# Kernel tuning notes

Measured on AMD Instinct MI355X. Metric: run time of the kernel, lower is better.

The kernel has to match this reference:

```python
import jax, jax.numpy as jnp
import numpy as np
from jax import lax

EPS = 1e-5

def setup_inputs() -> dict:
    key = jax.random.key(0)
    k1, k2 = jax.random.split(key)
    x = jax.random.normal(k1, (8, 256, 64, 64), dtype=jnp.float32)
    W = jax.random.normal(k2, (128, 256, 5, 5), dtype=jnp.float32) * 0.02
    gamma = jnp.ones((128,), dtype=jnp.float32)
    beta = jnp.zeros((128,), dtype=jnp.float32)
    return {"x": x, "W": W, "gamma": gamma, "beta": beta}

def reference(x, W, gamma, beta):
    B, C, H, Wd = x.shape
    # bilinear x2 upsample, half-pixel centers (== torch align_corners=False)
    up = jax.image.resize(x, (B, C, 2 * H, 2 * Wd), method="bilinear")
    # conv2d, stride 1, padding 2, no bias (norm == 'BN')
    out = lax.conv_general_dilated(
        up, W, window_strides=(1, 1), padding=[(2, 2), (2, 2)],
        dimension_numbers=("NCHW", "OIHW", "NCHW"))
    # BatchNorm2d (batch statistics, training-style refresh)
    mean = jnp.mean(out, axis=(0, 2, 3))
    var = jnp.var(out, axis=(0, 2, 3))
    inv = gamma / jnp.sqrt(var + EPS)
    out = (out - mean[None, :, None, None]) * inv[None, :, None, None] + beta[None, :, None, None]
    # activation: torch.relu
    return jax.nn.relu(out)
```

## Files before the change

### kernel.cpp

```cpp
#include <hip/hip_runtime.h>
#include <hip/hip_bf16.h>
#include <stdint.h>

typedef short s8v __attribute__((ext_vector_type(8)));
typedef float f4v __attribute__((ext_vector_type(4)));

__device__ __forceinline__ void async_copy16(const void* gsrc, void* lds_dst) {
  __builtin_amdgcn_global_load_lds(
      (const __attribute__((address_space(1))) uint32_t*)(uintptr_t)gsrc,
      (__attribute__((address_space(3))) uint32_t*)(uint32_t)(uintptr_t)lds_dst,
      16, 0, 0);
}

__global__ void wpack_kernel(const float* __restrict__ W, __hip_bfloat16* __restrict__ Wr) {
  int i = blockIdx.x * 256 + threadIdx.x;
  int ci = i & 255;
  int rest = i >> 8;
  int co = rest & 127;
  int pos = rest >> 7;
  Wr[i] = __float2bfloat16(W[(co * 256 + ci) * 25 + pos]);
}

__global__ __launch_bounds__(256, 2) void upsample_kernel(const float* __restrict__ x,
                                                          __hip_bfloat16* __restrict__ up) {
  __shared__ __hip_bfloat16 lx[10 * 48 * 66];
  const int tid = threadIdx.x;
  const int bx = blockIdx.x;
  const int owb = bx & 1;
  const int ohb = (bx >> 1) & 7;
  const int cb = (bx >> 4) & 3;
  const int b = bx >> 6;
  const int oh0 = ohb * 16, ow0 = owb * 64, c0 = cb * 64;
  const int ih0 = (oh0 >> 1) - 1;
  const int iw_lo = (ow0 >> 1) - 1;
  const int aligned = (iw_lo < 0 ? 0 : iw_lo) & ~15;

  for (int i = tid; i < 64 * 10 * 12; i += 256) {
    int c = i / 120;
    int rem = i - c * 120;
    int r = rem / 12;
    int w4 = (rem - r * 12) * 4;
    int gr = ih0 + r;
    gr = gr < 0 ? 0 : (gr > 63 ? 63 : gr);
    const float4 v = *(const float4*)&x[(((b * 256 + c0 + c) * 64) + gr) * 64 + aligned + w4];
    int base = (r * 48 + w4) * 66 + c;
    lx[base]       = __float2bfloat16(v.x);
    lx[base + 66]  = __float2bfloat16(v.y);
    lx[base + 132] = __float2bfloat16(v.z);
    lx[base + 198] = __float2bfloat16(v.w);
  }
  __syncthreads();

  const int c_l = tid & 63;
  const int owq = tid >> 6;
  for (int it = 0; it < 256; ++it) {
    int oh_l = it >> 4;
    int ow_l = (it & 15) * 4 + owq;
    int oh = oh0 + oh_l, ow = ow0 + ow_l;
    int ihA = (oh >> 1) - ((oh & 1) ^ 1);
    float wh = (oh & 1) ? 0.75f : 0.25f;
    int iwA = (ow >> 1) - ((ow & 1) ^ 1);
    float wwt = (ow & 1) ? 0.75f : 0.25f;
    int r0 = ihA - ih0;
    int w0 = (iwA < 0 ? 0 : iwA) - aligned;
    int w1t = iwA + 1; w1t = w1t > 63 ? 63 : w1t;
    int w1 = w1t - aligned;
    float t00 = __bfloat162float(lx[(r0 * 48 + w0) * 66 + c_l]);
    float t01 = __bfloat162float(lx[(r0 * 48 + w1) * 66 + c_l]);
    float t10 = __bfloat162float(lx[((r0 + 1) * 48 + w0) * 66 + c_l]);
    float t11 = __bfloat162float(lx[((r0 + 1) * 48 + w1) * 66 + c_l]);
    float v = wh * (wwt * t00 + (1.f - wwt) * t01) + (1.f - wh) * (wwt * t10 + (1.f - wwt) * t11);
    up[(((size_t)(b * 128 + oh) * 128) + ow) * 256 + c0 + c_l] = __float2bfloat16(v);
  }
}

#define SLOTC 1056
__global__ __launch_bounds__(512, 2) void conv_kernel(const __hip_bfloat16* __restrict__ up,
                                                      const __hip_bfloat16* __restrict__ Wr,
                                                      float* __restrict__ out,
                                                      float* __restrict__ gstats) {
  __shared__ __align__(16) unsigned short lA[6 * 132 * 64];
  __shared__ __align__(16) unsigned short lB[2][128 * 64];

  const int tid = threadIdx.x;
  const int lane = tid & 63;
  const int wave = tid >> 6;
  const int wm = wave >> 1;
  const int wn = wave & 1;
  const int lane15 = lane & 15;
  const int quad = lane >> 4;
  const int wb = wave << 6;

  const int bid = blockIdx.x;
  const int orig = ((bid & 7) << 5) | (bid >> 3);
  const int b = orig >> 5;
  const int oh0 = (orig & 31) << 2;

  const f4v zero4 = {0.f, 0.f, 0.f, 0.f};

  if (tid < 192) {
    int s = tid >> 5, j = tid & 31;
    int rsel = j >> 3;
    int r = (rsel < 2) ? rsel : (128 + rsel);
    *(f4v*)&lA[(s * SLOTC + r * 8 + (j & 7)) * 8] = zero4;
  }

  f4v acc[8][4];
#pragma unroll
  for (int i = 0; i < 8; ++i)
#pragma unroll
    for (int j = 0; j < 4; ++j) acc[i][j] = zero4;

  for (int rr = 0; rr < 4; ++rr) {
    int ih = oh0 + rr - 2;
    if ((unsigned)ih < 128u) {
      int sp = ih % 6;
      const __hip_bfloat16* uprow = up + (size_t)(b * 128 + ih) * 128 * 256;
#pragma unroll
      for (int t = 0; t < 2; ++t) {
        int pl = t * 512 + wb + lane;
        int riw = pl >> 3, pc = pl & 7;
        int cq = pc ^ ((riw + 2) & 7);
        async_copy16(uprow + riw * 256 + cq * 8,
                     (void*)&lA[(sp * SLOTC + 16 + t * 512 + wb) * 8]);
      }
    }
  }
#pragma unroll
  for (int t = 0; t < 2; ++t) {
    int pl = t * 512 + wb + lane;
    int n = pl >> 3, pc = pl & 7;
    int cq = pc ^ (n & 7);
    async_copy16(Wr + n * 256 + cq * 8, (void*)&lB[0][(t * 512 + wb) * 8]);
  }
  __syncthreads();

  int buf = 0;
  for (int cb = 0; cb < 4; ++cb) {
    const int c0 = cb << 6;
    for (int kh = 0; kh < 5; ++kh) {
      const int ih = oh0 + wm + kh - 2;
      const bool rowok = (unsigned)ih < 128u;
      const int abase = rowok ? (ih % 6) * SLOTC : 0;
      for (int kw = 0; kw < 5; ++kw) {
        const int pos = kh * 5 + kw;
        if (pos < 24) {
          const __hip_bfloat16* wrow = Wr + (size_t)(pos + 1) * 32768 + c0;
#pragma unroll
          for (int t = 0; t < 2; ++t) {
            int pl = t * 512 + wb + lane;
            int n = pl >> 3, pc = pl & 7;
            int cq = pc ^ (n & 7);
            async_copy16(wrow + n * 256 + cq * 8, (void*)&lB[buf ^ 1][(t * 512 + wb) * 8]);
          }
        }
        if (kw == 0 && kh < 4) {
          int ihp = oh0 + kh + 2;
          if (ihp < 128) {
            int sp = ihp % 6;
            const __hip_bfloat16* uprow = up + (size_t)(b * 128 + ihp) * 128 * 256 + c0;
#pragma unroll
            for (int t = 0; t < 2; ++t) {
              int pl = t * 512 + wb + lane;
              int riw = pl >> 3, pc = pl & 7;
              int cq = pc ^ ((riw + 2) & 7);
              async_copy16(uprow + riw * 256 + cq * 8,
                           (void*)&lA[(sp * SLOTC + 16 + t * 512 + wb) * 8]);
            }
          }
        }
        if (rowok) {
#pragma unroll
          for (int ks = 0; ks < 2; ++ks) {
            const int cq = ks * 4 + quad;
            s8v a[8], bb[4];
#pragma unroll
            for (int mt = 0; mt < 8; ++mt) {
              int r = mt * 16 + lane15 + kw;
              a[mt] = *(const s8v*)&lA[(abase + r * 8 + (cq ^ (r & 7))) * 8];
            }
#pragma unroll
            for (int nt = 0; nt < 4; ++nt) {
              int n = (wn << 6) + nt * 16 + lane15;
              bb[nt] = *(const s8v*)&lB[buf][(n * 8 + (cq ^ (n & 7))) * 8];
            }
#pragma unroll
            for (int mt = 0; mt < 8; ++mt)
#pragma unroll
              for (int nt = 0; nt < 4; ++nt)
                acc[mt][nt] = __builtin_amdgcn_mfma_f32_16x16x32_bf16(a[mt], bb[nt], acc[mt][nt], 0, 0, 0);
          }
        }
        __syncthreads();
        buf ^= 1;
      }
    }
    if (cb < 3) {
      const int c0n = (cb + 1) << 6;
      for (int rr = 0; rr < 4; ++rr) {
        int ihn = oh0 + rr - 2;
        if ((unsigned)ihn < 128u) {
          int sp = ihn % 6;
          const __hip_bfloat16* uprow = up + (size_t)(b * 128 + ihn) * 128 * 256 + c0n;
#pragma unroll
          for (int t = 0; t < 2; ++t) {
            int pl = t * 512 + wb + lane;
            int riw = pl >> 3, pc = pl & 7;
            int cq = pc ^ ((riw + 2) & 7);
            async_copy16(uprow + riw * 256 + cq * 8,
                         (void*)&lA[(sp * SLOTC + 16 + t * 512 + wb) * 8]);
          }
        }
      }
#pragma unroll
      for (int t = 0; t < 2; ++t) {
        int pl = t * 512 + wb + lane;
        int n = pl >> 3, pc = pl & 7;
        int cq = pc ^ (n & 7);
        async_copy16(Wr + c0n + n * 256 + cq * 8, (void*)&lB[buf ^ 1][(t * 512 + wb) * 8]);
      }
      __syncthreads();
      buf ^= 1;
    }
  }

  const int oh = oh0 + wm;
#pragma unroll
  for (int nt = 0; nt < 4; ++nt) {
    const int n = (wn << 6) + nt * 16 + lane15;
    float* oc = out + (((size_t)(b * 128 + n)) * 128 + oh) * 128;
    float s = 0.f, ss = 0.f;
#pragma unroll
    for (int mt = 0; mt < 8; ++mt) {
      f4v v = acc[mt][nt];
      *(f4v*)&oc[mt * 16 + (quad << 2)] = v;
      s += v.x + v.y + v.z + v.w;
      ss += v.x * v.x + v.y * v.y + v.z * v.z + v.w * v.w;
    }
    s += __shfl_xor(s, 16, 64); ss += __shfl_xor(ss, 16, 64);
    s += __shfl_xor(s, 32, 64); ss += __shfl_xor(ss, 32, 64);
    if (quad == 0) {
      atomicAdd(&gstats[n], s);
      atomicAdd(&gstats[128 + n], ss);
    }
  }
}

__global__ void scalebias_kernel(const float* __restrict__ gstats, const float* __restrict__ gamma,
                                 const float* __restrict__ beta, float* __restrict__ sb) {
  int c = threadIdx.x;
  float mean = gstats[c] * (1.f / 131072.f);
  float var = gstats[128 + c] * (1.f / 131072.f) - mean * mean;
  float inv = gamma[c] * rsqrtf(var + 1e-5f);
  sb[c] = inv;
  sb[128 + c] = beta[c] - mean * inv;
}

__global__ void norm_kernel(float* __restrict__ out, const float* __restrict__ sb) {
  int i = blockIdx.x * 256 + threadIdx.x;
  f4v v = ((f4v*)out)[i];
  int c = (i >> 12) & 127;
  float sc = sb[c], bi = sb[128 + c];
  v.x = fmaxf(fmaf(v.x, sc, bi), 0.f);
  v.y = fmaxf(fmaf(v.y, sc, bi), 0.f);
  v.z = fmaxf(fmaf(v.z, sc, bi), 0.f);
  v.w = fmaxf(fmaf(v.w, sc, bi), 0.f);
  ((f4v*)out)[i] = v;
}

extern "C" void kernel_launch(void* const* d_in, const int* in_sizes, int n_in,
                              void* d_out, int out_size, void* d_ws, size_t ws_size,
                              hipStream_t stream) {
  (void)in_sizes; (void)n_in; (void)out_size; (void)ws_size;
  const float* x = (const float*)d_in[0];
  const float* W = (const float*)d_in[1];
  const float* gamma = (const float*)d_in[2];
  const float* beta = (const float*)d_in[3];
  float* out = (float*)d_out;
  char* ws = (char*)d_ws;
  __hip_bfloat16* up = (__hip_bfloat16*)ws;
  __hip_bfloat16* Wr = (__hip_bfloat16*)(ws + 67108864);
  float* gstats = (float*)(ws + 67108864 + 1638400);
  float* sb = gstats + 256;

  hipMemsetAsync(gstats, 0, 256 * sizeof(float), stream);
  wpack_kernel<<<3200, 256, 0, stream>>>(W, Wr);
  upsample_kernel<<<512, 256, 0, stream>>>(x, up);
  conv_kernel<<<256, 512, 0, stream>>>(up, Wr, out, gstats);
  scalebias_kernel<<<1, 128, 0, stream>>>(gstats, gamma, beta, sb);
  norm_kernel<<<16384, 256, 0, stream>>>(out, sb);
}
```

Measured before the change: 333.7 us.

## Split conv tiles along width, shrink LDS ring, pair-vectorize upsample

The conv kernel now splits each output row block into two 64-wide halves, doubling the grid to 512 blocks. Per-block accumulators and the LDS A ring shrink (5 slots with halo and zero-padded edges via a global zeros buffer) so launch bounds allow 4 blocks per CU. It also merges the next-channel-block weight prefetch into the kw loop and reduces BN stats in LDS before the global atomics. The upsample kernel processes two channels per thread with 32-bit LDS loads and packed stores. The trade-off is that the halo rows are loaded twice and there is extra per-block overhead.

```diff
diff --git a/kernel.cpp b/kernel.cpp
--- a/kernel.cpp
+++ b/kernel.cpp
@@ -4,6 +4,8 @@
 
 typedef short s8v __attribute__((ext_vector_type(8)));
 typedef float f4v __attribute__((ext_vector_type(4)));
+
+__device__ __align__(16) float g_zeros[4] = {0.f, 0.f, 0.f, 0.f};
 
 __device__ __forceinline__ void async_copy16(const void* gsrc, void* lds_dst) {
   __builtin_amdgcn_global_load_lds(
@@ -51,11 +53,12 @@
   }
   __syncthreads();
 
-  const int c_l = tid & 63;
-  const int owq = tid >> 6;
-  for (int it = 0; it < 256; ++it) {
-    int oh_l = it >> 4;
-    int ow_l = (it & 15) * 4 + owq;
+  const int c2 = (tid & 31) * 2;
+  const int owq = tid >> 5;
+  uint32_t* upu = (uint32_t*)up;
+  for (int it = 0; it < 128; ++it) {
+    int oh_l = it >> 3;
+    int ow_l = (it & 7) * 8 + owq;
     int oh = oh0 + oh_l, ow = ow0 + ow_l;
     int ihA = (oh >> 1) - ((oh & 1) ^ 1);
     float wh = (oh & 1) ? 0.75f : 0.25f;
@@ -65,22 +68,31 @@
     int w0 = (iwA < 0 ? 0 : iwA) - aligned;
     int w1t = iwA + 1; w1t = w1t > 63 ? 63 : w1t;
     int w1 = w1t - aligned;
-    float t00 = __bfloat162float(lx[(r0 * 48 + w0) * 66 + c_l]);
-    float t01 = __bfloat162float(lx[(r0 * 48 + w1) * 66 + c_l]);
-    float t10 = __bfloat162float(lx[((r0 + 1) * 48 + w0) * 66 + c_l]);
-    float t11 = __bfloat162float(lx[((r0 + 1) * 48 + w1) * 66 + c_l]);
-    float v = wh * (wwt * t00 + (1.f - wwt) * t01) + (1.f - wh) * (wwt * t10 + (1.f - wwt) * t11);
-    up[(((size_t)(b * 128 + oh) * 128) + ow) * 256 + c0 + c_l] = __float2bfloat16(v);
-  }
-}
-
-#define SLOTC 1056
-__global__ __launch_bounds__(512, 2) void conv_kernel(const __hip_bfloat16* __restrict__ up,
+    uint32_t t00 = *(const uint32_t*)&lx[(r0 * 48 + w0) * 66 + c2];
+    uint32_t t01 = *(const uint32_t*)&lx[(r0 * 48 + w1) * 66 + c2];
+    uint32_t t10 = *(const uint32_t*)&lx[((r0 + 1) * 48 + w0) * 66 + c2];
+    uint32_t t11 = *(const uint32_t*)&lx[((r0 + 1) * 48 + w1) * 66 + c2];
+    float wlo = wh * wwt, wlo1 = wh * (1.f - wwt);
+    float whi = (1.f - wh) * wwt, whi1 = (1.f - wh) * (1.f - wwt);
+    float vlo = wlo * __uint_as_float(t00 << 16) + wlo1 * __uint_as_float(t01 << 16) +
+                whi * __uint_as_float(t10 << 16) + whi1 * __uint_as_float(t11 << 16);
+    float vhi = wlo * __uint_as_float(t00 & 0xffff0000u) + wlo1 * __uint_as_float(t01 & 0xffff0000u) +
+                whi * __uint_as_float(t10 & 0xffff0000u) + whi1 * __uint_as_float(t11 & 0xffff0000u);
+    __hip_bfloat16 h0 = __float2bfloat16(vlo);
+    __hip_bfloat16 h1 = __float2bfloat16(vhi);
+    uint32_t pk = (uint32_t)(*(unsigned short*)&h0) | ((uint32_t)(*(unsigned short*)&h1) << 16);
+    upu[((((size_t)(b * 128 + oh) * 128) + ow) * 256 + c0 + c2) >> 1] = pk;
+  }
+}
+
+#define ASLOT 4608
+__global__ __launch_bounds__(512, 4) void conv_kernel(const __hip_bfloat16* __restrict__ up,
                                                       const __hip_bfloat16* __restrict__ Wr,
                                                       float* __restrict__ out,
                                                       float* __restrict__ gstats) {
-  __shared__ __align__(16) unsigned short lA[6 * 132 * 64];
+  __shared__ __align__(16) unsigned short lA[5 * ASLOT];
   __shared__ __align__(16) unsigned short lB[2][128 * 64];
+  __shared__ float lsum[128], lssq[128];
 
   const int tid = threadIdx.x;
   const int lane = tid & 63;
@@ -89,50 +101,69 @@
   const int wn = wave & 1;
   const int lane15 = lane & 15;
   const int quad = lane >> 4;
-  const int wb = wave << 6;
 
   const int bid = blockIdx.x;
-  const int orig = ((bid & 7) << 5) | (bid >> 3);
-  const int b = orig >> 5;
-  const int oh0 = (orig & 31) << 2;
+  const int orig = ((bid & 7) << 6) | (bid >> 3);
+  const int b = orig >> 6;
+  const int oh0 = ((orig >> 1) & 31) << 2;
+  const int owh = orig & 1;
+  const int ow0 = owh << 6;
 
   const f4v zero4 = {0.f, 0.f, 0.f, 0.f};
-
-  if (tid < 192) {
-    int s = tid >> 5, j = tid & 31;
-    int rsel = j >> 3;
-    int r = (rsel < 2) ? rsel : (128 + rsel);
-    *(f4v*)&lA[(s * SLOTC + r * 8 + (j & 7)) * 8] = zero4;
-  }
-
-  f4v acc[8][4];
-#pragma unroll
-  for (int i = 0; i < 8; ++i)
+  if (tid < 128) { lsum[tid] = 0.f; lssq[tid] = 0.f; }
+  if (owh == 0) {
+    for (int i = tid; i < 5 * 32; i += 512) {
+      int s = i >> 5, rem = i & 31;
+      *(f4v*)&lA[(s * 576 + (rem >> 3) * 8 + (rem & 7)) * 8] = zero4;
+    }
+  } else {
+    for (int i = tid; i < 5 * 48; i += 512) {
+      int s = i / 48, rem = i - s * 48;
+      *(f4v*)&lA[(s * 576 + (66 + (rem >> 3)) * 8 + (rem & 7)) * 8] = zero4;
+    }
+  }
+
+  auto stageA = [&](int slot, const __hip_bfloat16* uprow) {
+    int idx = (wave << 6) + lane;
+    int r = idx >> 3, pc = idx & 7;
+    int cq = pc ^ (r & 7);
+    int iw = ow0 - 4 + r;
+    const void* src = ((unsigned)iw < 128u) ? (const void*)(uprow + iw * 256 + cq * 8)
+                                            : (const void*)g_zeros;
+    async_copy16(src, (void*)&lA[(slot * 576 + (wave << 6)) * 8]);
+    if (wave == 0) {
+      int idx2 = 512 + lane;
+      int r2 = idx2 >> 3, pc2 = idx2 & 7;
+      int cq2 = pc2 ^ (r2 & 7);
+      int iw2 = ow0 - 4 + r2;
+      const void* src2 = ((unsigned)iw2 < 128u) ? (const void*)(uprow + iw2 * 256 + cq2 * 8)
+                                                : (const void*)g_zeros;
+      async_copy16(src2, (void*)&lA[(slot * 576 + 512) * 8]);
+    }
+  };
+  auto stageB = [&](const __hip_bfloat16* wrow, int bsel) {
+#pragma unroll
+    for (int t = 0; t < 2; ++t) {
+      int base = t * 512 + (wave << 6);
+      int idx = base + lane;
+      int n = idx >> 3, pc = idx & 7;
+      int cq = pc ^ (n & 7);
+      async_copy16(wrow + n * 256 + cq * 8, (void*)&lB[bsel][base * 8]);
+    }
+  };
+
+  f4v acc[4][4];
+#pragma unroll
+  for (int i = 0; i < 4; ++i)
 #pragma unroll
     for (int j = 0; j < 4; ++j) acc[i][j] = zero4;
 
   for (int rr = 0; rr < 4; ++rr) {
     int ih = oh0 + rr - 2;
-    if ((unsigned)ih < 128u) {
-      int sp = ih % 6;
-      const __hip_bfloat16* uprow = up + (size_t)(b * 128 + ih) * 128 * 256;
-#pragma unroll
-      for (int t = 0; t < 2; ++t) {
-        int pl = t * 512 + wb + lane;
-        int riw = pl >> 3, pc = pl & 7;
-        int cq = pc ^ ((riw + 2) & 7);
-        async_copy16(uprow + riw * 256 + cq * 8,
-                     (void*)&lA[(sp * SLOTC + 16 + t * 512 + wb) * 8]);
-      }
-    }
-  }
-#pragma unroll
-  for (int t = 0; t < 2; ++t) {
-    int pl = t * 512 + wb + lane;
-    int n = pl >> 3, pc = pl & 7;
-    int cq = pc ^ (n & 7);
-    async_copy16(Wr + n * 256 + cq * 8, (void*)&lB[0][(t * 512 + wb) * 8]);
-  }
+    if ((unsigned)ih < 128u)
+      stageA(ih % 5, up + (size_t)(b * 128 + ih) * 128 * 256);
+  }
+  stageB(Wr, 0);
   __syncthreads();
 
   int buf = 0;
@@ -141,43 +172,28 @@
     for (int kh = 0; kh < 5; ++kh) {
       const int ih = oh0 + wm + kh - 2;
       const bool rowok = (unsigned)ih < 128u;
-      const int abase = rowok ? (ih % 6) * SLOTC : 0;
+      const int abase = rowok ? (ih % 5) * ASLOT : 0;
       for (int kw = 0; kw < 5; ++kw) {
         const int pos = kh * 5 + kw;
         if (pos < 24) {
-          const __hip_bfloat16* wrow = Wr + (size_t)(pos + 1) * 32768 + c0;
-#pragma unroll
-          for (int t = 0; t < 2; ++t) {
-            int pl = t * 512 + wb + lane;
-            int n = pl >> 3, pc = pl & 7;
-            int cq = pc ^ (n & 7);
-            async_copy16(wrow + n * 256 + cq * 8, (void*)&lB[buf ^ 1][(t * 512 + wb) * 8]);
-          }
+          stageB(Wr + (size_t)(pos + 1) * 32768 + c0, buf ^ 1);
+        } else if (cb < 3) {
+          stageB(Wr + (c0 + 64), buf ^ 1);
         }
-        if (kw == 0 && kh < 4) {
+        if (kw == 2 && kh < 4) {
           int ihp = oh0 + kh + 2;
-          if (ihp < 128) {
-            int sp = ihp % 6;
-            const __hip_bfloat16* uprow = up + (size_t)(b * 128 + ihp) * 128 * 256 + c0;
-#pragma unroll
-            for (int t = 0; t < 2; ++t) {
-              int pl = t * 512 + wb + lane;
-              int riw = pl >> 3, pc = pl & 7;
-              int cq = pc ^ ((riw + 2) & 7);
-              async_copy16(uprow + riw * 256 + cq * 8,
-                           (void*)&lA[(sp * SLOTC + 16 + t * 512 + wb) * 8]);
-            }
-          }
+          if (ihp < 128)
+            stageA(ihp % 5, up + (size_t)(b * 128 + ihp) * 128 * 256 + c0);
         }
         if (rowok) {
 #pragma unroll
           for (int ks = 0; ks < 2; ++ks) {
             const int cq = ks * 4 + quad;
-            s8v a[8], bb[4];
-#pragma unroll
-            for (int mt = 0; mt < 8; ++mt) {
-              int r = mt * 16 + lane15 + kw;
-              a[mt] = *(const s8v*)&lA[(abase + r * 8 + (cq ^ (r & 7))) * 8];
+            s8v a[4], bb[4];
+#pragma unroll
+            for (int mt = 0; mt < 4; ++mt) {
+              int r = mt * 16 + lane15 + kw + 2;
+              a[mt] = *(const s8v*)&lA[abase + (r * 8 + (cq ^ (r & 7))) * 8];
             }
 #pragma unroll
             for (int nt = 0; nt < 4; ++nt) {
@@ -185,7 +201,7 @@
               bb[nt] = *(const s8v*)&lB[buf][(n * 8 + (cq ^ (n & 7))) * 8];
             }
 #pragma unroll
-            for (int mt = 0; mt < 8; ++mt)
+            for (int mt = 0; mt < 4; ++mt)
 #pragma unroll
               for (int nt = 0; nt < 4; ++nt)
                 acc[mt][nt] = __builtin_amdgcn_mfma_f32_16x16x32_bf16(a[mt], bb[nt], acc[mt][nt], 0, 0, 0);
@@ -199,28 +215,10 @@
       const int c0n = (cb + 1) << 6;
       for (int rr = 0; rr < 4; ++rr) {
         int ihn = oh0 + rr - 2;
-        if ((unsigned)ihn < 128u) {
-          int sp = ihn % 6;
-          const __hip_bfloat16* uprow = up + (size_t)(b * 128 + ihn) * 128 * 256 + c0n;
-#pragma unroll
-          for (int t = 0; t < 2; ++t) {
-            int pl = t * 512 + wb + lane;
-            int riw = pl >> 3, pc = pl & 7;
-            int cq = pc ^ ((riw + 2) & 7);
-            async_copy16(uprow + riw * 256 + cq * 8,
-                         (void*)&lA[(sp * SLOTC + 16 + t * 512 + wb) * 8]);
-          }
-        }
-      }
-#pragma unroll
-      for (int t = 0; t < 2; ++t) {
-        int pl = t * 512 + wb + lane;
-        int n = pl >> 3, pc = pl & 7;
-        int cq = pc ^ (n & 7);
-        async_copy16(Wr + c0n + n * 256 + cq * 8, (void*)&lB[buf ^ 1][(t * 512 + wb) * 8]);
+        if ((unsigned)ihn < 128u)
+          stageA(ihn % 5, up + (size_t)(b * 128 + ihn) * 128 * 256 + c0n);
       }
       __syncthreads();
-      buf ^= 1;
     }
   }
 
@@ -228,10 +226,10 @@
 #pragma unroll
   for (int nt = 0; nt < 4; ++nt) {
     const int n = (wn << 6) + nt * 16 + lane15;
-    float* oc = out + (((size_t)(b * 128 + n)) * 128 + oh) * 128;
+    float* oc = out + ((size_t)(b * 128 + n) * 128 + oh) * 128 + ow0;
     float s = 0.f, ss = 0.f;
 #pragma unroll
-    for (int mt = 0; mt < 8; ++mt) {
+    for (int mt = 0; mt < 4; ++mt) {
       f4v v = acc[mt][nt];
       *(f4v*)&oc[mt * 16 + (quad << 2)] = v;
       s += v.x + v.y + v.z + v.w;
@@ -239,10 +237,12 @@
     }
     s += __shfl_xor(s, 16, 64); ss += __shfl_xor(ss, 16, 64);
     s += __shfl_xor(s, 32, 64); ss += __shfl_xor(ss, 32, 64);
-    if (quad == 0) {
-      atomicAdd(&gstats[n], s);
-      atomicAdd(&gstats[128 + n], ss);
-    }
+    if (quad == 0) { atomicAdd(&lsum[n], s); atomicAdd(&lssq[n], ss); }
+  }
+  __syncthreads();
+  if (tid < 128) {
+    atomicAdd(&gstats[tid], lsum[tid]);
+    atomicAdd(&gstats[128 + tid], lssq[tid]);
   }
 }
 
@@ -286,7 +286,7 @@
   hipMemsetAsync(gstats, 0, 256 * sizeof(float), stream);
   wpack_kernel<<<3200, 256, 0, stream>>>(W, Wr);
   upsample_kernel<<<512, 256, 0, stream>>>(x, up);
-  conv_kernel<<<256, 512, 0, stream>>>(up, Wr, out, gstats);
+  conv_kernel<<<512, 512, 0, stream>>>(up, Wr, out, gstats);
   scalebias_kernel<<<1, 128, 0, stream>>>(gstats, gamma, beta, sb);
   norm_kernel<<<16384, 256, 0, stream>>>(out, sb);
 }
```

Result: no change. 339.0 us (+1.6%).
